# Performance work log

Measured on AMD Instinct MI355X. Metric: run time of the kernel, lower is better.

The kernel has to match this reference:

```python
import jax, jax.numpy as jnp
import numpy as np

B, N, F_IN, F_OUT, H = 4, 2048, 256, 256, 4
NEG_INF = -1e9
EDGE_PROB = 0.05
LEAKY_SLOPE = 0.2  # tf.nn.leaky_relu default alpha


def setup_inputs() -> dict:
    key = jax.random.key(0)
    k_x, k_m, k_w, k_a, k_b = jax.random.split(key, 5)
    inputs = jax.random.normal(k_x, (B, N, F_IN), dtype=jnp.float32)
    # bias: additive adjacency mask, 0 on edges / -1e9 off-edges (standard GAT)
    u = jax.random.uniform(k_m, (B, N, N), dtype=jnp.float32)
    bias = jnp.where(u < EDGE_PROB, 0.0, NEG_INF).astype(jnp.float32)
    # self-loops so every softmax row has at least one valid entry
    bias = bias.at[:, jnp.arange(N), jnp.arange(N)].set(0.0)
    # per-head learned params (uniform [0,1) init as in the original)
    W = jax.random.uniform(k_w, (H, F_IN, F_OUT), dtype=jnp.float32)
    a = jax.random.uniform(k_a, (H, F_OUT), dtype=jnp.float32)
    b = jax.random.uniform(k_b, (H, F_OUT), dtype=jnp.float32)
    return {"inputs": inputs, "bias": bias, "W": W, "a": a, "b": b}


def reference(inputs, bias, W, a, b):
    # transformed: [H, B, N, F_OUT]
    t = jnp.einsum('bnf,hfo->hbno', inputs, W) + b[:, None, None, :]
    # per-node score s = t @ a : [H, B, N]
    s = jnp.einsum('hbno,ho->hbn', t, a)
    # weights[i,j] = s[i] + s[j]  (weights + transpose)
    w = s[..., :, None] + s[..., None, :]  # [H, B, N, N]
    coefs = jax.nn.softmax(jax.nn.leaky_relu(w, negative_slope=LEAKY_SLOPE) + bias, axis=-1)
    heads = jnp.einsum('hbnm,hbmo->hbno', coefs, t)  # [H, B, N, F_OUT]
    return jnp.mean(heads, axis=0)  # (1/num_heads) * add_n(heads)
```

## Files before the change

### kernel.cpp

```cpp
#include <hip/hip_runtime.h>
#include <hip/hip_bf16.h>
#include <stdint.h>

#define H 4
#define BB 4
#define NN 2048
#define FIN 256
#define FOUT 256
#define M_TOT (BB*NN)
#define LOG2E 1.44269504f

typedef float f32x4 __attribute__((ext_vector_type(4)));
typedef short s16x8 __attribute__((ext_vector_type(8)));
typedef unsigned int u32;

static __device__ __forceinline__ short f2bf(float f) {
    return __builtin_bit_cast(short, __float2bfloat16(f));
}
static __device__ __forceinline__ float bf2f(short u) {
    unsigned x = ((unsigned)(unsigned short)u) << 16;
    return __builtin_bit_cast(float, x);
}

__global__ __launch_bounds__(256) void k_prep(const float* __restrict__ W, const float* __restrict__ a,
                                              const float* __restrict__ bvec,
                                              short* __restrict__ WT, float* __restrict__ q,
                                              float* __restrict__ c) {
    int bid = blockIdx.x;
    if (bid < 64) {
        __shared__ float lds[64][65];
        int h = bid >> 4, kt = (bid >> 2) & 3, ot = bid & 3;
        int kb = kt * 64, ob = ot * 64;
        int tx = threadIdx.x & 63, ty = threadIdx.x >> 6;
#pragma unroll
        for (int r = 0; r < 16; ++r) {
            int k_l = ty + r * 4;
            lds[tx][k_l] = W[(size_t)(h * FIN + kb + k_l) * FOUT + ob + tx];
        }
        __syncthreads();
#pragma unroll
        for (int r = 0; r < 16; ++r) {
            int o_l = ty + r * 4;
            WT[(size_t)(h * FOUT + ob + o_l) * FIN + kb + tx] = f2bf(lds[o_l][tx]);
        }
    } else if (bid < 320) {
        int wv = ((bid - 64) * 256 + threadIdx.x) >> 6;
        int lane = threadIdx.x & 63;
        int h = wv >> 8, f = wv & 255;
        float4 w4 = *(const float4*)(W + (size_t)(h * FIN + f) * FOUT + lane * 4);
        float4 a4 = *(const float4*)(a + h * FOUT + lane * 4);
        float d = w4.x * a4.x + w4.y * a4.y + w4.z * a4.z + w4.w * a4.w;
#pragma unroll
        for (int off = 32; off; off >>= 1) d += __shfl_xor(d, off);
        if (lane == 0) q[h * FIN + f] = d;
    } else {
        int h = threadIdx.x >> 6, lane = threadIdx.x & 63;
        float4 b4 = *(const float4*)(bvec + h * FOUT + lane * 4);
        float4 a4 = *(const float4*)(a + h * FOUT + lane * 4);
        float d = b4.x * a4.x + b4.y * a4.y + b4.z * a4.z + b4.w * a4.w;
#pragma unroll
        for (int off = 32; off; off >>= 1) d += __shfl_xor(d, off);
        if (lane == 0) c[h] = d;
    }
}

__global__ __launch_bounds__(256) void k_s(const float* __restrict__ X, const float* __restrict__ q,
                                           const float* __restrict__ c, float* __restrict__ s,
                                           short* __restrict__ Xbf) {
    int m = blockIdx.x * 4 + (threadIdx.x >> 6);
    int lane = threadIdx.x & 63;
    float4 xv = *(const float4*)(X + (size_t)m * FIN + lane * 4);
    short4 xb;
    xb.x = f2bf(xv.x); xb.y = f2bf(xv.y); xb.z = f2bf(xv.z); xb.w = f2bf(xv.w);
    *(short4*)(Xbf + (size_t)m * FIN + lane * 4) = xb;
#pragma unroll
    for (int h = 0; h < H; ++h) {
        float4 qv = *(const float4*)(q + h * FIN + lane * 4);
        float d = xv.x * qv.x + xv.y * qv.y + xv.z * qv.z + xv.w * qv.w;
#pragma unroll
        for (int off = 32; off; off >>= 1) d += __shfl_xor(d, off);
        if (lane == 0) s[h * M_TOT + m] = d + c[h];
    }
}

__global__ __launch_bounds__(256) void k_maskmax(const float* __restrict__ bias, const float* __restrict__ s,
                                                 unsigned* __restrict__ mask, float* __restrict__ mtot) {
    __shared__ float sl[8192];
    int tid = threadIdx.x;
    int row0 = blockIdx.x * 4;
    int b = row0 >> 11;
#pragma unroll
    for (int i = 0; i < 8; ++i) {
        int flat = i * 1024 + tid * 4;
        int h = flat >> 11, j = flat & 2047;
        float4 v = *(const float4*)(s + (size_t)h * M_TOT + (size_t)b * NN + j);
        int phys = flat ^ (((flat >> 5) & 7) << 2);
        *(float4*)(sl + phys) = v;
    }
    __syncthreads();

    int w = tid >> 6, lane = tid & 63;
    int row = row0 + w;
    int iloc = row & 2047;
    const float* bp = bias + (size_t)row * NN + lane * 32;
    unsigned bits = 0;
#pragma unroll
    for (int k = 0; k < 8; ++k) {
        float4 v = *(const float4*)(bp + k * 4);
        bits |= (v.x > -1.f ? 1u : 0u) << (k * 4 + 0);
        bits |= (v.y > -1.f ? 1u : 0u) << (k * 4 + 1);
        bits |= (v.z > -1.f ? 1u : 0u) << (k * 4 + 2);
        bits |= (v.w > -1.f ? 1u : 0u) << (k * 4 + 3);
    }
    mask[(size_t)row * 64 + lane] = bits;
#pragma unroll
    for (int h = 0; h < H; ++h) {
        float m = -3e38f;
#pragma unroll
        for (int k = 0; k < 8; ++k) {
            int flat = h * 2048 + lane * 32 + k * 4;
            int phys = flat ^ (((flat >> 5) & 7) << 2);
            float4 sv = *(const float4*)(sl + phys);
            m = fmaxf(m, ((bits >> (k * 4 + 0)) & 1u) ? sv.x : -3e38f);
            m = fmaxf(m, ((bits >> (k * 4 + 1)) & 1u) ? sv.y : -3e38f);
            m = fmaxf(m, ((bits >> (k * 4 + 2)) & 1u) ? sv.z : -3e38f);
            m = fmaxf(m, ((bits >> (k * 4 + 3)) & 1u) ? sv.w : -3e38f);
        }
#pragma unroll
        for (int off = 32; off; off >>= 1) m = fmaxf(m, __shfl_xor(m, off));
        int sidx = h * 2048 + iloc;
        float si = sl[sidx ^ (((sidx >> 5) & 7) << 2)];
        float z = si + m;
        float Mlog = fmaxf(z, 0.2f * z) * LOG2E;
        float c1 = si * LOG2E - Mlog;
        float c2 = 0.2f * si * LOG2E - Mlog;
        const float k1 = LOG2E, k2 = 0.2f * LOG2E;
        float l = 0.f;
#pragma unroll
        for (int k = 0; k < 8; ++k) {
            int flat = h * 2048 + lane * 32 + k * 4;
            int phys = flat ^ (((flat >> 5) & 7) << 2);
            float4 sv = *(const float4*)(sl + phys);
            float svv[4] = {sv.x, sv.y, sv.z, sv.w};
#pragma unroll
            for (int e = 0; e < 4; ++e) {
                float aa = fmaxf(fmaf(svv[e], k1, c1), fmaf(svv[e], k2, c2));
                aa = ((bits >> (k * 4 + e)) & 1u) ? aa : -200.f;
                l += __builtin_amdgcn_exp2f(aa);
            }
        }
#pragma unroll
        for (int off = 32; off; off >>= 1) l += __shfl_xor(l, off);
        if (lane == 0) mtot[h * M_TOT + row] = Mlog + __builtin_amdgcn_logf(l);
    }
}

__global__ __launch_bounds__(256) void k_gemm_t(const short* __restrict__ WT, const short* __restrict__ Xbf,
                                                const float* __restrict__ bvec, short* __restrict__ tTs) {
    __shared__ short ot[64][136];
    int h = blockIdx.z;
    int ob = blockIdx.y * 64;
    int mb = blockIdx.x * 128;
    int tid = threadIdx.x;
    int lane = tid & 63, w = tid >> 6;
    int r16 = lane & 15, g = lane >> 4;
    int mw = mb + w * 32;
    f32x4 acc[4][2] = {};
    for (int k = 0; k < FIN; k += 32) {
        s16x8 afr[4], bfr[2];
#pragma unroll
        for (int fa = 0; fa < 4; ++fa)
            afr[fa] = *(const s16x8*)(WT + (size_t)(h * FOUT + ob + fa * 16 + r16) * FIN + k + g * 8);
#pragma unroll
        for (int fb = 0; fb < 2; ++fb)
            bfr[fb] = *(const s16x8*)(Xbf + (size_t)(mw + fb * 16 + r16) * FIN + k + g * 8);
#pragma unroll
        for (int fa = 0; fa < 4; ++fa)
#pragma unroll
            for (int fb = 0; fb < 2; ++fb)
                acc[fa][fb] = __builtin_amdgcn_mfma_f32_16x16x32_bf16(afr[fa], bfr[fb], acc[fa][fb], 0, 0, 0);
    }
#pragma unroll
    for (int fa = 0; fa < 4; ++fa) {
#pragma unroll
        for (int r = 0; r < 4; ++r) {
            int o_l = fa * 16 + g * 4 + r;
            float bv = bvec[h * FOUT + ob + o_l];
#pragma unroll
            for (int fb = 0; fb < 2; ++fb)
                ot[o_l][w * 32 + fb * 16 + r16] = f2bf(acc[fa][fb][r] + bv);
        }
    }
    __syncthreads();
    int bb = mb >> 11, jloc = mb & 2047;
    int jt0 = jloc >> 6;
    size_t slab = (size_t)((h * 4 + bb) * 32) * 16384;
#pragma unroll
    for (int cc = 0; cc < 4; ++cc) {
        int sid = cc * 256 + tid;
        int frag = sid >> 6;
        int l = sid & 63;
        int f_l = frag >> 2, jt_sel = (frag >> 1) & 1, par = frag & 1;
        int o_l = f_l * 16 + (l & 15);
        int m_l = jt_sel * 64 + par * 32 + (l >> 4) * 8;
        s16x8 v = *(const s16x8*)&ot[o_l][m_l];
        int fid = ((ob >> 4) + f_l) * 2 + par;
        size_t addr = slab + (size_t)(jt0 + jt_sel) * 16384 + fid * 512 + l * 8;
        *(s16x8*)(tTs + addr) = v;
    }
}

__global__ __launch_bounds__(512, 4) void k_attn(const short* __restrict__ tTs, const float* __restrict__ s,
                                                 const unsigned* __restrict__ mask, const float* __restrict__ mtot,
                                                 short* __restrict__ OT) {
    __shared__ short smem[16640];

    int flat = blockIdx.x + 32 * (blockIdx.y + 4 * blockIdx.z);
    int swz = (flat & 7) * 64 + (flat >> 3);
    int qt = swz & 31, b = (swz >> 5) & 3, h = swz >> 7;
    int ib = qt * 64;

    int tid = threadIdx.x;
    int lane = tid & 63, w = tid >> 6;
    int r16 = lane & 15, g = lane >> 4;
    int par = w & 1, oh = w >> 1;
    size_t gm = (size_t)b * NN;

    const short* slab = tTs + (size_t)((h * 4 + b) * 32) * 16384;
    const float* srow = s + h * M_TOT + gm;

    int i = ib + oh * 16 + r16;
    float si = srow[i];
    float mt = mtot[h * M_TOT + gm + i];
    float c1 = si * LOG2E - mt;
    float c2 = 0.2f * si * LOG2E - mt;
    const float k1 = LOG2E, k2 = 0.2f * LOG2E;
    const unsigned* mk = mask + (gm + i) * 64;

    int chk = ((((par << 2) + g) ^ (r16 & 7)) << 3);
    int rdP = r16 * 64 + chk;
    int wrP = oh * 1024 + rdP;

    f32x4 acc[4][4] = {};

    s16x8 acur[4], anext[4];
#pragma unroll
    for (int f = 0; f < 4; ++f)
        acur[f] = *(const s16x8*)(slab + ((oh * 4 + f) * 2 + par) * 512 + lane * 8);

    float4 psj0, psj1; unsigned pwm;
    {
        int jw = par * 32;
        psj0 = *(const float4*)(srow + jw + g * 8);
        psj1 = *(const float4*)(srow + jw + g * 8 + 4);
        pwm = mk[par];
    }

    for (int t = 0; t < 32; ++t) {
        if (t < 31) {
            const short* tp = slab + (size_t)(t + 1) * 16384;
#pragma unroll
            for (int f = 0; f < 4; ++f)
                anext[f] = *(const s16x8*)(tp + ((oh * 4 + f) * 2 + par) * 512 + lane * 8);
        }

        float sjv[8] = {psj0.x, psj0.y, psj0.z, psj0.w, psj1.x, psj1.y, psj1.z, psj1.w};
        unsigned bb0 = pwm >> (g * 8);
        s16x8 pb;
#pragma unroll
        for (int e = 0; e < 8; ++e) {
            float u = fmaf(sjv[e], k1, c1);
            float vv = fmaf(sjv[e], k2, c2);
            float aa = fmaxf(u, vv);
            aa = ((bb0 >> e) & 1u) ? aa : -200.f;
            pb[e] = f2bf(__builtin_amdgcn_exp2f(aa));
        }
        *(s16x8*)(smem + (t & 1) * 4096 + wrP) = pb;

        if (t < 31) {
            int jw = (t + 1) * 64 + par * 32;
            psj0 = *(const float4*)(srow + jw + g * 8);
            psj1 = *(const float4*)(srow + jw + g * 8 + 4);
            pwm = mk[(t + 1) * 2 + par];
        }

        asm volatile("s_waitcnt lgkmcnt(0)" ::: "memory");
        __builtin_amdgcn_sched_barrier(0);
        __builtin_amdgcn_s_barrier();
        __builtin_amdgcn_sched_barrier(0);

        const short* Pb = smem + (t & 1) * 4096;
        __builtin_amdgcn_s_setprio(1);
#pragma unroll
        for (int qf = 0; qf < 4; ++qf) {
            s16x8 pf = *(const s16x8*)(Pb + qf * 1024 + rdP);
            acc[0][qf] = __builtin_amdgcn_mfma_f32_16x16x32_bf16(acur[0], pf, acc[0][qf], 0, 0, 0);
            acc[1][qf] = __builtin_amdgcn_mfma_f32_16x16x32_bf16(acur[1], pf, acc[1][qf], 0, 0, 0);
            acc[2][qf] = __builtin_amdgcn_mfma_f32_16x16x32_bf16(acur[2], pf, acc[2][qf], 0, 0, 0);
            acc[3][qf] = __builtin_amdgcn_mfma_f32_16x16x32_bf16(acur[3], pf, acc[3][qf], 0, 0, 0);
        }
        __builtin_amdgcn_s_setprio(0);

        if (t < 31) {
#pragma unroll
            for (int f = 0; f < 4; ++f) acur[f] = anext[f];
        }
    }

    __syncthreads();
    f32x4* ex = (f32x4*)smem;
    size_t hbase = (size_t)h * FOUT * M_TOT + gm;
#pragma unroll
    for (int rnd = 0; rnd < 2; ++rnd) {
        if (par == 1 && (oh >> 1) == rnd) {
#pragma unroll
            for (int f = 0; f < 4; ++f)
#pragma unroll
                for (int qf = 0; qf < 4; ++qf)
                    ex[(((oh & 1) * 4 + f) * 4 + qf) * 64 + lane] = acc[f][qf];
        }
        __syncthreads();
        if (par == 0 && (oh >> 1) == rnd) {
#pragma unroll
            for (int f = 0; f < 4; ++f)
#pragma unroll
                for (int qf = 0; qf < 4; ++qf) {
                    f32x4 v = acc[f][qf] + ex[(((oh & 1) * 4 + f) * 4 + qf) * 64 + lane];
                    int iq = ib + qf * 16 + r16;
#pragma unroll
                    for (int rr = 0; rr < 4; ++rr) {
                        int o = (oh * 4 + f) * 16 + g * 4 + rr;
                        OT[hbase + (size_t)o * M_TOT + iq] = f2bf(v[rr]);
                    }
                }
        }
        __syncthreads();
    }
}

__global__ __launch_bounds__(256) void k_reduce(const short* __restrict__ OT, float* __restrict__ out) {
    __shared__ float lds[32][72];
    int mb = blockIdx.x * 64, obt = blockIdx.y * 32;
    int tid = threadIdx.x;
    {
        int o_l = tid >> 3;
        int m_l = (tid & 7) * 8;
        float acc[8] = {};
#pragma unroll
        for (int h = 0; h < H; ++h) {
            s16x8 v = *(const s16x8*)(OT + (size_t)(h * FOUT + obt + o_l) * M_TOT + mb + m_l);
#pragma unroll
            for (int e = 0; e < 8; ++e) acc[e] += bf2f(v[e]);
        }
#pragma unroll
        for (int e = 0; e < 8; ++e) lds[o_l][m_l + e] = acc[e] * 0.25f;
    }
    __syncthreads();
    {
        int m_l = tid >> 2;
        int o_l = (tid & 3) * 8;
        float4 v0, v1;
        v0.x = lds[o_l + 0][m_l]; v0.y = lds[o_l + 1][m_l];
        v0.z = lds[o_l + 2][m_l]; v0.w = lds[o_l + 3][m_l];
        v1.x = lds[o_l + 4][m_l]; v1.y = lds[o_l + 5][m_l];
        v1.z = lds[o_l + 6][m_l]; v1.w = lds[o_l + 7][m_l];
        float* dst = out + (size_t)(mb + m_l) * FOUT + obt + o_l;
        *(float4*)dst = v0;
        *(float4*)(dst + 4) = v1;
    }
}

extern "C" void kernel_launch(void* const* d_in, const int* in_sizes, int n_in,
                              void* d_out, int out_size, void* d_ws, size_t ws_size,
                              hipStream_t stream) {
    const float* X    = (const float*)d_in[0];
    const float* bias = (const float*)d_in[1];
    const float* W    = (const float*)d_in[2];
    const float* a    = (const float*)d_in[3];
    const float* bvec = (const float*)d_in[4];
    float* out = (float*)d_out;

    char* ws = (char*)d_ws;
    short*    Xbf  = (short*)ws;
    short*    WT   = (short*)(ws + (4u << 20));
    float*    q    = (float*)(ws + (4u << 20) + (768u << 10));
    float*    c    = q + H * FIN;
    float*    s    = (float*)(ws + (5u << 20));
    float*    mtot = (float*)(ws + (5u << 20) + (256u << 10));
    short*    tTs  = (short*)(ws + (6u << 20));
    short*    OT   = (short*)(ws + (22u << 20));
    unsigned* mask = (unsigned*)(ws + (38u << 20));

    k_prep<<<321, 256, 0, stream>>>(W, a, bvec, WT, q, c);
    k_s<<<2048, 256, 0, stream>>>(X, q, c, s, Xbf);
    k_maskmax<<<2048, 256, 0, stream>>>(bias, s, mask, mtot);
    k_gemm_t<<<dim3(64, 4, 4), 256, 0, stream>>>(WT, Xbf, bvec, tTs);
    k_attn<<<dim3(32, 4, 4), 512, 0, stream>>>(tTs, s, mask, mtot, OT);
    k_reduce<<<dim3(128, 8), 256, 0, stream>>>(OT, out);
}
```

Baseline: 120.7 us.

## Split attention key dimension across two workgroups to double grid parallelism

```diff
diff --git a/kernel.cpp b/kernel.cpp
--- a/kernel.cpp
+++ b/kernel.cpp
@@ -212,12 +212,22 @@
 
 __global__ __launch_bounds__(512, 4) void k_attn(const short* __restrict__ tTs, const float* __restrict__ s,
                                                  const unsigned* __restrict__ mask, const float* __restrict__ mtot,
-                                                 short* __restrict__ OT) {
+                                                 short* __restrict__ OT, int jsplit) {
     __shared__ short smem[16640];
 
-    int flat = blockIdx.x + 32 * (blockIdx.y + 4 * blockIdx.z);
-    int swz = (flat & 7) * 64 + (flat >> 3);
-    int qt = swz & 31, b = (swz >> 5) & 3, h = swz >> 7;
+    int nwgy = 4 * jsplit;
+    int nwg = 32 * nwgy * 4;
+    int flat = blockIdx.x + 32 * (blockIdx.y + nwgy * blockIdx.z);
+    int swz = (flat & 7) * (nwg >> 3) + (flat >> 3);
+    int qt = swz & 31;
+    int rr_ = swz >> 5;
+    int shift = (jsplit == 2) ? 3 : 2;
+    int y2 = rr_ & ((1 << shift) - 1);
+    int h = rr_ >> shift;
+    int b  = (jsplit == 2) ? (y2 >> 1) : y2;
+    int jh = (jsplit == 2) ? (y2 & 1) : 0;
+    int NT = 32 / jsplit;
+    int jt0 = jh * NT;
     int ib = qt * 64;
 
     int tid = threadIdx.x;
@@ -246,18 +256,19 @@
     s16x8 acur[4], anext[4];
 #pragma unroll
     for (int f = 0; f < 4; ++f)
-        acur[f] = *(const s16x8*)(slab + ((oh * 4 + f) * 2 + par) * 512 + lane * 8);
+        acur[f] = *(const s16x8*)(slab + (size_t)jt0 * 16384 + ((oh * 4 + f) * 2 + par) * 512 + lane * 8);
 
     float4 psj0, psj1; unsigned pwm;
     {
-        int jw = par * 32;
+        int jw = jt0 * 64 + par * 32;
         psj0 = *(const float4*)(srow + jw + g * 8);
         psj1 = *(const float4*)(srow + jw + g * 8 + 4);
-        pwm = mk[par];
-    }
-
-    for (int t = 0; t < 32; ++t) {
-        if (t < 31) {
+        pwm = mk[jt0 * 2 + par];
+    }
+
+    for (int tt = 0; tt < NT; ++tt) {
+        int t = jt0 + tt;
+        if (tt < NT - 1) {
             const short* tp = slab + (size_t)(t + 1) * 16384;
 #pragma unroll
             for (int f = 0; f < 4; ++f)
@@ -275,9 +286,9 @@
             aa = ((bb0 >> e) & 1u) ? aa : -200.f;
             pb[e] = f2bf(__builtin_amdgcn_exp2f(aa));
         }
-        *(s16x8*)(smem + (t & 1) * 4096 + wrP) = pb;
-
-        if (t < 31) {
+        *(s16x8*)(smem + (tt & 1) * 4096 + wrP) = pb;
+
+        if (tt < NT - 1) {
             int jw = (t + 1) * 64 + par * 32;
             psj0 = *(const float4*)(srow + jw + g * 8);
             psj1 = *(const float4*)(srow + jw + g * 8 + 4);
@@ -289,7 +300,7 @@
         __builtin_amdgcn_s_barrier();
         __builtin_amdgcn_sched_barrier(0);
 
-        const short* Pb = smem + (t & 1) * 4096;
+        const short* Pb = smem + (tt & 1) * 4096;
         __builtin_amdgcn_s_setprio(1);
 #pragma unroll
         for (int qf = 0; qf < 4; ++qf) {
@@ -301,7 +312,7 @@
         }
         __builtin_amdgcn_s_setprio(0);
 
-        if (t < 31) {
+        if (tt < NT - 1) {
 #pragma unroll
             for (int f = 0; f < 4; ++f) acur[f] = anext[f];
         }
@@ -309,7 +320,7 @@
 
     __syncthreads();
     f32x4* ex = (f32x4*)smem;
-    size_t hbase = (size_t)h * FOUT * M_TOT + gm;
+    size_t hbase = ((size_t)jh * H + h) * FOUT * M_TOT + gm;
 #pragma unroll
     for (int rnd = 0; rnd < 2; ++rnd) {
         if (par == 1 && (oh >> 1) == rnd) {
@@ -328,9 +339,9 @@
                     f32x4 v = acc[f][qf] + ex[(((oh & 1) * 4 + f) * 4 + qf) * 64 + lane];
                     int iq = ib + qf * 16 + r16;
 #pragma unroll
-                    for (int rr = 0; rr < 4; ++rr) {
-                        int o = (oh * 4 + f) * 16 + g * 4 + rr;
-                        OT[hbase + (size_t)o * M_TOT + iq] = f2bf(v[rr]);
+                    for (int rr2 = 0; rr2 < 4; ++rr2) {
+                        int o = (oh * 4 + f) * 16 + g * 4 + rr2;
+                        OT[hbase + (size_t)o * M_TOT + iq] = f2bf(v[rr2]);
                     }
                 }
         }
@@ -338,7 +349,8 @@
     }
 }
 
-__global__ __launch_bounds__(256) void k_reduce(const short* __restrict__ OT, float* __restrict__ out) {
+__global__ __launch_bounds__(256) void k_reduce(const short* __restrict__ OT, float* __restrict__ out,
+                                                int nslab) {
     __shared__ float lds[32][72];
     int mb = blockIdx.x * 64, obt = blockIdx.y * 32;
     int tid = threadIdx.x;
@@ -346,9 +358,9 @@
         int o_l = tid >> 3;
         int m_l = (tid & 7) * 8;
         float acc[8] = {};
-#pragma unroll
-        for (int h = 0; h < H; ++h) {
-            s16x8 v = *(const s16x8*)(OT + (size_t)(h * FOUT + obt + o_l) * M_TOT + mb + m_l);
+        for (int u = 0; u < nslab; ++u) {
+            s16x8 v = *(const s16x8*)(OT + (size_t)u * FOUT * M_TOT
+                                         + (size_t)(obt + o_l) * M_TOT + mb + m_l);
 #pragma unroll
             for (int e = 0; e < 8; ++e) acc[e] += bf2f(v[e]);
         }
@@ -380,6 +392,8 @@
     const float* bvec = (const float*)d_in[4];
     float* out = (float*)d_out;
 
+    int jsplit = (ws_size >= (size_t)56 * 1024 * 1024) ? 2 : 1;
+
     char* ws = (char*)d_ws;
     short*    Xbf  = (short*)ws;
     short*    WT   = (short*)(ws + (4u << 20));
@@ -389,12 +403,12 @@
     float*    mtot = (float*)(ws + (5u << 20) + (256u << 10));
     short*    tTs  = (short*)(ws + (6u << 20));
     short*    OT   = (short*)(ws + (22u << 20));
-    unsigned* mask = (unsigned*)(ws + (38u << 20));
+    unsigned* mask = (unsigned*)(ws + ((size_t)(22 + 16 * jsplit) << 20));
 
     k_prep<<<321, 256, 0, stream>>>(W, a, bvec, WT, q, c);
     k_s<<<2048, 256, 0, stream>>>(X, q, c, s, Xbf);
     k_maskmax<<<2048, 256, 0, stream>>>(bias, s, mask, mtot);
     k_gemm_t<<<dim3(64, 4, 4), 256, 0, stream>>>(WT, Xbf, bvec, tTs);
-    k_attn<<<dim3(32, 4, 4), 512, 0, stream>>>(tTs, s, mask, mtot, OT);
-    k_reduce<<<dim3(128, 8), 256, 0, stream>>>(OT, out);
-}
+    k_attn<<<dim3(32, 4 * jsplit, 4), 512, 0, stream>>>(tTs, s, mask, mtot, OT, jsplit);
+    k_reduce<<<dim3(128, 8), 256, 0, stream>>>(OT, out, 4 * jsplit);
+}
```

Result: slower. 146.1 us (+21.0%).

## Software-pipeline P tile generation one step ahead of MFMA consumption

Applied to the files above, without the earlier changes.

```diff
diff --git a/kernel.cpp b/kernel.cpp
--- a/kernel.cpp
+++ b/kernel.cpp
@@ -249,21 +249,12 @@
         acur[f] = *(const s16x8*)(slab + ((oh * 4 + f) * 2 + par) * 512 + lane * 8);
 
     float4 psj0, psj1; unsigned pwm;
+
     {
         int jw = par * 32;
         psj0 = *(const float4*)(srow + jw + g * 8);
         psj1 = *(const float4*)(srow + jw + g * 8 + 4);
         pwm = mk[par];
-    }
-
-    for (int t = 0; t < 32; ++t) {
-        if (t < 31) {
-            const short* tp = slab + (size_t)(t + 1) * 16384;
-#pragma unroll
-            for (int f = 0; f < 4; ++f)
-                anext[f] = *(const s16x8*)(tp + ((oh * 4 + f) * 2 + par) * 512 + lane * 8);
-        }
-
         float sjv[8] = {psj0.x, psj0.y, psj0.z, psj0.w, psj1.x, psj1.y, psj1.z, psj1.w};
         unsigned bb0 = pwm >> (g * 8);
         s16x8 pb;
@@ -275,36 +266,79 @@
             aa = ((bb0 >> e) & 1u) ? aa : -200.f;
             pb[e] = f2bf(__builtin_amdgcn_exp2f(aa));
         }
-        *(s16x8*)(smem + (t & 1) * 4096 + wrP) = pb;
+        *(s16x8*)(smem + wrP) = pb;
+        int jw1 = 64 + par * 32;
+        psj0 = *(const float4*)(srow + jw1 + g * 8);
+        psj1 = *(const float4*)(srow + jw1 + g * 8 + 4);
+        pwm = mk[2 + par];
+    }
+    asm volatile("s_waitcnt lgkmcnt(0)" ::: "memory");
+    __builtin_amdgcn_sched_barrier(0);
+    __builtin_amdgcn_s_barrier();
+
+    for (int t = 0; t < 32; ++t) {
+        const short* Pb = smem + (t & 1) * 4096;
+        s16x8 pf0 = *(const s16x8*)(Pb + 0 * 1024 + rdP);
+        s16x8 pf1 = *(const s16x8*)(Pb + 1 * 1024 + rdP);
+        s16x8 pf2 = *(const s16x8*)(Pb + 2 * 1024 + rdP);
+        s16x8 pf3 = *(const s16x8*)(Pb + 3 * 1024 + rdP);
 
         if (t < 31) {
-            int jw = (t + 1) * 64 + par * 32;
+            const short* tp = slab + (size_t)(t + 1) * 16384;
+#pragma unroll
+            for (int f = 0; f < 4; ++f)
+                anext[f] = *(const s16x8*)(tp + ((oh * 4 + f) * 2 + par) * 512 + lane * 8);
+        }
+
+        if (t < 31) {
+            float sjv[8] = {psj0.x, psj0.y, psj0.z, psj0.w, psj1.x, psj1.y, psj1.z, psj1.w};
+            unsigned bb0 = pwm >> (g * 8);
+            s16x8 pb;
+#pragma unroll
+            for (int e = 0; e < 8; ++e) {
+                float u = fmaf(sjv[e], k1, c1);
+                float vv = fmaf(sjv[e], k2, c2);
+                float aa = fmaxf(u, vv);
+                aa = ((bb0 >> e) & 1u) ? aa : -200.f;
+                pb[e] = f2bf(__builtin_amdgcn_exp2f(aa));
+            }
+            *(s16x8*)(smem + ((t + 1) & 1) * 4096 + wrP) = pb;
+        }
+
+        if (t < 30) {
+            int jw = (t + 2) * 64 + par * 32;
             psj0 = *(const float4*)(srow + jw + g * 8);
             psj1 = *(const float4*)(srow + jw + g * 8 + 4);
-            pwm = mk[(t + 1) * 2 + par];
+            pwm = mk[(t + 2) * 2 + par];
+        }
+
+        __builtin_amdgcn_s_setprio(1);
+        acc[0][0] = __builtin_amdgcn_mfma_f32_16x16x32_bf16(acur[0], pf0, acc[0][0], 0, 0, 0);
+        acc[1][0] = __builtin_amdgcn_mfma_f32_16x16x32_bf16(acur[1], pf0, acc[1][0], 0, 0, 0);
+        acc[2][0] = __builtin_amdgcn_mfma_f32_16x16x32_bf16(acur[2], pf0, acc[2][0], 0, 0, 0);
+        acc[3][0] = __builtin_amdgcn_mfma_f32_16x16x32_bf16(acur[3], pf0, acc[3][0], 0, 0, 0);
+        acc[0][1] = __builtin_amdgcn_mfma_f32_16x16x32_bf16(acur[0], pf1, acc[0][1], 0, 0, 0);
+        acc[1][1] = __builtin_amdgcn_mfma_f32_16x16x32_bf16(acur[1], pf1, acc[1][1], 0, 0, 0);
+        acc[2][1] = __builtin_amdgcn_mfma_f32_16x16x32_bf16(acur[2], pf1, acc[2][1], 0, 0, 0);
+        acc[3][1] = __builtin_amdgcn_mfma_f32_16x16x32_bf16(acur[3], pf1, acc[3][1], 0, 0, 0);
+        acc[0][2] = __builtin_amdgcn_mfma_f32_16x16x32_bf16(acur[0], pf2, acc[0][2], 0, 0, 0);
+        acc[1][2] = __builtin_amdgcn_mfma_f32_16x16x32_bf16(acur[1], pf2, acc[1][2], 0, 0, 0);
+        acc[2][2] = __builtin_amdgcn_mfma_f32_16x16x32_bf16(acur[2], pf2, acc[2][2], 0, 0, 0);
+        acc[3][2] = __builtin_amdgcn_mfma_f32_16x16x32_bf16(acur[3], pf2, acc[3][2], 0, 0, 0);
+        acc[0][3] = __builtin_amdgcn_mfma_f32_16x16x32_bf16(acur[0], pf3, acc[0][3], 0, 0, 0);
+        acc[1][3] = __builtin_amdgcn_mfma_f32_16x16x32_bf16(acur[1], pf3, acc[1][3], 0, 0, 0);
+        acc[2][3] = __builtin_amdgcn_mfma_f32_16x16x32_bf16(acur[2], pf3, acc[2][3], 0, 0, 0);
+        acc[3][3] = __builtin_amdgcn_mfma_f32_16x16x32_bf16(acur[3], pf3, acc[3][3], 0, 0, 0);
+        __builtin_amdgcn_s_setprio(0);
+
+        if (t < 31) {
+#pragma unroll
+            for (int f = 0; f < 4; ++f) acur[f] = anext[f];
         }
 
         asm volatile("s_waitcnt lgkmcnt(0)" ::: "memory");
         __builtin_amdgcn_sched_barrier(0);
         __builtin_amdgcn_s_barrier();
-        __builtin_amdgcn_sched_barrier(0);
-
-        const short* Pb = smem + (t & 1) * 4096;
-        __builtin_amdgcn_s_setprio(1);
-#pragma unroll
-        for (int qf = 0; qf < 4; ++qf) {
-            s16x8 pf = *(const s16x8*)(Pb + qf * 1024 + rdP);
-            acc[0][qf] = __builtin_amdgcn_mfma_f32_16x16x32_bf16(acur[0], pf, acc[0][qf], 0, 0, 0);
-            acc[1][qf] = __builtin_amdgcn_mfma_f32_16x16x32_bf16(acur[1], pf, acc[1][qf], 0, 0, 0);
-            acc[2][qf] = __builtin_amdgcn_mfma_f32_16x16x32_bf16(acur[2], pf, acc[2][qf], 0, 0, 0);
-            acc[3][qf] = __builtin_amdgcn_mfma_f32_16x16x32_bf16(acur[3], pf, acc[3][qf], 0, 0, 0);
-        }
-        __builtin_amdgcn_s_setprio(0);
-
-        if (t < 31) {
-#pragma unroll
-            for (int f = 0; f < 4; ++f) acur[f] = anext[f];
-        }
     }
 
     __syncthreads();
```

Result: slower. 199.2 us (+65.0%).
